# Optimization experiments

Measured on AMD Instinct MI355X. Metric: run time of the kernel, lower is better.

Reference implementation:

```python
import jax, jax.numpy as jnp
import numpy as np

EMBED_DIM = 1024
NUM_HEADS = 16
HEAD_DIM = EMBED_DIM // NUM_HEADS
B, SQ, SKV = 2, 2048, 2048


def setup_inputs() -> dict:
    key = jax.random.key(0)
    ks = jax.random.split(key, 12)
    s = 1.0 / np.sqrt(EMBED_DIM)
    inp = {
        "query": jax.random.normal(ks[0], (B, SQ, EMBED_DIM), jnp.float32),
        "key": jax.random.normal(ks[1], (B, SKV, EMBED_DIM), jnp.float32),
        "value": jax.random.normal(ks[2], (B, SKV, EMBED_DIM), jnp.float32),
        "Wq": jax.random.normal(ks[3], (EMBED_DIM, EMBED_DIM), jnp.float32) * s,
        "bq": jnp.zeros((EMBED_DIM,), jnp.float32),
        "Wk": jax.random.normal(ks[4], (EMBED_DIM, EMBED_DIM), jnp.float32) * s,
        "bk": jnp.zeros((EMBED_DIM,), jnp.float32),
        "Wv": jax.random.normal(ks[5], (EMBED_DIM, EMBED_DIM), jnp.float32) * s,
        "bv": jnp.zeros((EMBED_DIM,), jnp.float32),
        "Wo": jax.random.normal(ks[6], (EMBED_DIM, EMBED_DIM), jnp.float32) * s,
        "bo": jnp.zeros((EMBED_DIM,), jnp.float32),
        "ln_gamma": jnp.ones((EMBED_DIM,), jnp.float32),
        "ln_beta": jnp.zeros((EMBED_DIM,), jnp.float32),
    }
    return inp


def reference(query, key, value, Wq, bq, Wk, bk, Wv, bv, Wo, bo, ln_gamma, ln_beta):
    b, sq, d = query.shape
    skv = key.shape[1]
    residual = query
    # projections -> [b, h, s, hd]
    Q = (query @ Wq + bq).reshape(b, sq, NUM_HEADS, HEAD_DIM).transpose(0, 2, 1, 3)
    K = (key @ Wk + bk).reshape(b, skv, NUM_HEADS, HEAD_DIM).transpose(0, 2, 1, 3)
    V = (value @ Wv + bv).reshape(b, skv, NUM_HEADS, HEAD_DIM).transpose(0, 2, 1, 3)
    scores = jnp.einsum("bhqd,bhkd->bhqk", Q, K) / jnp.sqrt(jnp.float32(HEAD_DIM)).astype(Q.dtype)
    attn = jax.nn.softmax(scores, axis=-1)  # dropout identity in eval
    attended = jnp.einsum("bhqk,bhkd->bhqd", attn, V)
    attended = attended.transpose(0, 2, 1, 3).reshape(b, sq, d)
    out = attended @ Wo + bo
    x = out + residual
    mu = jnp.mean(x, axis=-1, keepdims=True)
    var = jnp.var(x, axis=-1, keepdims=True)
    return (x - mu) / jnp.sqrt(var + 1e-5) * ln_gamma + ln_beta
```

## Files before the change

kernel.cpp:

```cpp
#include <hip/hip_runtime.h>

#define EMBED 1024
#define NHEAD 16
#define HDIM  64
#define BATCH 2
#define SEQ   2048
#define ROWS  (BATCH*SEQ)

typedef __bf16 bf16x8 __attribute__((ext_vector_type(8)));
typedef float  f32x4  __attribute__((ext_vector_type(4)));
typedef float  f32x16 __attribute__((ext_vector_type(16)));
typedef unsigned short u16x8 __attribute__((ext_vector_type(8)));
typedef unsigned short u16x4 __attribute__((ext_vector_type(4)));
typedef unsigned int   u32x2 __attribute__((ext_vector_type(2)));

__device__ __forceinline__ unsigned short f2bf(float f) {
    unsigned int u = __float_as_uint(f);
    u += 0x7FFFu + ((u >> 16) & 1u);
    return (unsigned short)(u >> 16);
}
__device__ __forceinline__ f32x4 zero4() { f32x4 z = {0.f, 0.f, 0.f, 0.f}; return z; }

__device__ __forceinline__ unsigned int cvtpk_bf16(float lo, float hi) {
    unsigned int r;
    asm("v_cvt_pk_bf16_f32 %0, %1, %2" : "=v"(r) : "v"(lo), "v"(hi));
    return r;
}
__device__ __forceinline__ void pl32swap(unsigned int &a, unsigned int &b) {
    asm("v_permlane32_swap_b32 %0, %1" : "+v"(a), "+v"(b));
}
__device__ __forceinline__ float exp2_hw(float x) {
    float r;
    asm("v_exp_f32 %0, %1" : "=v"(r) : "v"(x));
    return r;
}

__device__ __forceinline__ void gl_lds16(const unsigned short* g, unsigned short* l) {
    __builtin_amdgcn_global_load_lds(
        (const __attribute__((address_space(1))) void*)g,
        (__attribute__((address_space(3))) void*)l, 16, 0, 0);
}

__global__ __launch_bounds__(256) void cvt3_kernel(const float* __restrict__ q,
                                                   const float* __restrict__ k,
                                                   const float* __restrict__ v,
                                                   unsigned short* __restrict__ qo,
                                                   unsigned short* __restrict__ ko,
                                                   unsigned short* __restrict__ vo) {
    const float* in; unsigned short* out;
    if (blockIdx.y == 0)      { in = q; out = qo; }
    else if (blockIdx.y == 1) { in = k; out = ko; }
    else                      { in = v; out = vo; }
    int i = (blockIdx.x * 256 + threadIdx.x) * 4;
    float4 vv = *(const float4*)(in + i);
    u16x4 o = {f2bf(vv.x), f2bf(vv.y), f2bf(vv.z), f2bf(vv.w)};
    *(u16x4*)(out + i) = o;
}

__global__ __launch_bounds__(256) void transpose4_kernel(const float* __restrict__ w0,
                                                         const float* __restrict__ w1,
                                                         const float* __restrict__ w2,
                                                         const float* __restrict__ w3,
                                                         unsigned short* __restrict__ o0,
                                                         unsigned short* __restrict__ o1,
                                                         unsigned short* __restrict__ o2,
                                                         unsigned short* __restrict__ o3) {
    const float* in; unsigned short* out;
    if (blockIdx.z == 0)      { in = w0; out = o0; }
    else if (blockIdx.z == 1) { in = w1; out = o1; }
    else if (blockIdx.z == 2) { in = w2; out = o2; }
    else                      { in = w3; out = o3; }
    __shared__ float tile[32][33];
    int tx = threadIdx.x, ty = threadIdx.y;
    int x = blockIdx.x * 32 + tx;
    int y0 = blockIdx.y * 32 + ty;
#pragma unroll
    for (int r = 0; r < 4; ++r)
        tile[ty + 8 * r][tx] = in[(size_t)(y0 + 8 * r) * EMBED + x];
    __syncthreads();
    int ox = blockIdx.y * 32 + tx;
    int oy = blockIdx.x * 32 + ty;
#pragma unroll
    for (int r = 0; r < 4; ++r)
        out[(size_t)(oy + 8 * r) * EMBED + ox] = f2bf(tile[tx][ty + 8 * r]);
}

__global__ __launch_bounds__(256, 2) void gemm_qkv_kernel(
    const unsigned short* __restrict__ qb, const unsigned short* __restrict__ kb,
    const unsigned short* __restrict__ vb,
    const unsigned short* __restrict__ Wqt, const unsigned short* __restrict__ Wkt,
    const unsigned short* __restrict__ Wvt,
    const float* __restrict__ bq, const float* __restrict__ bk, const float* __restrict__ bv,
    unsigned short* __restrict__ Qp, unsigned short* __restrict__ Kp,
    unsigned short* __restrict__ Vtb) {
    __shared__ unsigned short smem[16384];
    const unsigned short *A, *Bt; const float* bias; unsigned short* outp; int mode; float osc;
    if (blockIdx.z == 0)      { A = qb; Bt = Wqt; bias = bq; outp = Qp;  mode = 0; osc = 0.18033688f; }
    else if (blockIdx.z == 1) { A = kb; Bt = Wkt; bias = bk; outp = Kp;  mode = 0; osc = 1.0f; }
    else                      { A = vb; Bt = Wvt; bias = bv; outp = Vtb; mode = 1; osc = 1.0f; }

    const int t = threadIdx.x;
    const int m0 = blockIdx.x * 128, n0 = blockIdx.y * 128;
    const int wave = t >> 6, lane = t & 63;
    const int wr = wave >> 1, wc = wave & 1;
    const int lm = lane & 15, lq = lane >> 4;
    const int sr = t >> 2;
    const int csrc = (t & 3) ^ ((sr >> 1) & 3);
    const int pa = lq ^ ((lm >> 1) & 3);

    const unsigned short* gA = A + (size_t)(m0 + sr) * EMBED + csrc * 8;
    const unsigned short* gB = Bt + (size_t)(n0 + sr) * EMBED + csrc * 8;

    f32x4 acc[4][4];
#pragma unroll
    for (int i = 0; i < 4; ++i)
#pragma unroll
        for (int j = 0; j < 4; ++j) acc[i][j] = zero4();

    gl_lds16(gA,              smem + wave * 512);
    gl_lds16(gA + 64 * EMBED, smem + 2048 + wave * 512);
    gl_lds16(gB,              smem + 8192 + wave * 512);
    gl_lds16(gB + 64 * EMBED, smem + 8192 + 2048 + wave * 512);
    gA += 32; gB += 32;
    gl_lds16(gA,              smem + 4096 + wave * 512);
    gl_lds16(gA + 64 * EMBED, smem + 4096 + 2048 + wave * 512);
    gl_lds16(gB,              smem + 8192 + 4096 + wave * 512);
    gl_lds16(gB + 64 * EMBED, smem + 8192 + 4096 + 2048 + wave * 512);
    gA += 32; gB += 32;

    for (int kk = 0; kk < 32; ++kk) {
        if (kk < 31) { asm volatile("s_waitcnt vmcnt(4)" ::: "memory"); }
        else         { asm volatile("s_waitcnt vmcnt(0)" ::: "memory"); }
        __builtin_amdgcn_s_barrier();
        const int cbo = (kk & 1) * 4096;
        bf16x8 af[4], bfr[4];
#pragma unroll
        for (int i = 0; i < 4; ++i)
            af[i] = *(const bf16x8*)&smem[cbo + (wr * 64 + i * 16 + lm) * 32 + pa * 8];
#pragma unroll
        for (int j = 0; j < 4; ++j)
            bfr[j] = *(const bf16x8*)&smem[8192 + cbo + (wc * 64 + j * 16 + lm) * 32 + pa * 8];
#pragma unroll
        for (int i = 0; i < 4; ++i)
#pragma unroll
            for (int j = 0; j < 4; ++j)
                acc[i][j] = __builtin_amdgcn_mfma_f32_16x16x32_bf16(af[i], bfr[j], acc[i][j], 0, 0, 0);
        if (kk < 30) {
            __builtin_amdgcn_s_barrier();
            gl_lds16(gA,              smem + cbo + wave * 512);
            gl_lds16(gA + 64 * EMBED, smem + cbo + 2048 + wave * 512);
            gl_lds16(gB,              smem + 8192 + cbo + wave * 512);
            gl_lds16(gB + 64 * EMBED, smem + 8192 + cbo + 2048 + wave * 512);
            gA += 32; gB += 32;
        }
    }

    const int row = t >> 2, seg = t & 3;
    if (mode == 0) {
#pragma unroll
        for (int p = 0; p < 2; ++p) {
            __syncthreads();
            if (wr == p) {
#pragma unroll
                for (int i = 0; i < 4; ++i)
#pragma unroll
                    for (int j = 0; j < 4; ++j) {
                        float bn = bias[n0 + wc * 64 + j * 16 + lm];
                        int nl = wc * 64 + j * 16 + lm;
#pragma unroll
                        for (int r = 0; r < 4; ++r)
                            smem[(i * 16 + lq * 4 + r) * 136 + nl] =
                                f2bf((acc[i][j][r] + bn) * osc);
                    }
            }
            __syncthreads();
            int m = m0 + p * 64 + row;
            int b = m >> 11, sI = m & 2047;
            int ncol = n0 + seg * 32;
            int h = ncol >> 6, hd0 = ncol & 63;
            unsigned short* dst = outp + (((size_t)((b * NHEAD + h) * SEQ + sI)) << 6) + hd0;
            const unsigned short* src = smem + row * 136 + seg * 32;
            *(u16x8*)(dst)      = *(const u16x8*)(src);
            *(u16x8*)(dst + 8)  = *(const u16x8*)(src + 8);
            *(u16x8*)(dst + 16) = *(const u16x8*)(src + 16);
            *(u16x8*)(dst + 24) = *(const u16x8*)(src + 24);
        }
    } else {
#pragma unroll
        for (int p = 0; p < 2; ++p) {
            __syncthreads();
            if (wc == p) {
#pragma unroll
                for (int i = 0; i < 4; ++i)
#pragma unroll
                    for (int j = 0; j < 4; ++j) {
                        float bn = bias[n0 + p * 64 + j * 16 + lm];
                        u16x4 pw = {f2bf(acc[i][j][0] + bn), f2bf(acc[i][j][1] + bn),
                                    f2bf(acc[i][j][2] + bn), f2bf(acc[i][j][3] + bn)};
                        *(u16x4*)&smem[(j * 16 + lm) * 136 + wr * 64 + i * 16 + lq * 4] = pw;
                    }
            }
            __syncthreads();
            int n = n0 + p * 64 + row;
            int h = n >> 6, hd = n & 63;
            int b = m0 >> 11;
            int s0 = (m0 & 2047) + seg * 32;
            unsigned short* dst = outp + ((size_t)((b * NHEAD + h) * HDIM + hd)) * SEQ + s0;
            const unsigned short* src = smem + row * 136 + seg * 32;
            *(u16x8*)(dst)      = *(const u16x8*)(src);
            *(u16x8*)(dst + 8)  = *(const u16x8*)(src + 8);
            *(u16x8*)(dst + 16) = *(const u16x8*)(src + 16);
            *(u16x8*)(dst + 24) = *(const u16x8*)(src + 24);
        }
    }
}

__global__ __launch_bounds__(256, 2) void gemm_o_kernel(
    const unsigned short* __restrict__ att, const unsigned short* __restrict__ Wot,
    const float* __restrict__ bo, float* __restrict__ xbuf,
    const float* __restrict__ residual) {
    __shared__ unsigned short As[2][2048];
    __shared__ unsigned short Bs[2][4096];
    const int t = threadIdx.x;
    const int m0 = blockIdx.x * 64, n0 = blockIdx.y * 128;
    const int wave = t >> 6, lane = t & 63;
    const int lm = lane & 15, lq = lane >> 4;
    const int sr = t >> 2;
    const int csrc = (t & 3) ^ ((sr >> 1) & 3);
    const int pa = lq ^ ((lm >> 1) & 3);

    const unsigned short* gA = att + (size_t)(m0 + sr) * EMBED + csrc * 8;
    const unsigned short* gB = Wot + (size_t)(n0 + sr) * EMBED + csrc * 8;

    f32x4 acc[4][2];
#pragma unroll
    for (int i = 0; i < 4; ++i)
#pragma unroll
        for (int j = 0; j < 2; ++j) acc[i][j] = zero4();

    gl_lds16(gA,              As[0] + wave * 512);
    gl_lds16(gB,              Bs[0] + wave * 512);
    gl_lds16(gB + 64 * EMBED, Bs[0] + 2048 + wave * 512);
    gA += 32; gB += 32;
    gl_lds16(gA,              As[1] + wave * 512);
    gl_lds16(gB,              Bs[1] + wave * 512);
    gl_lds16(gB + 64 * EMBED, Bs[1] + 2048 + wave * 512);
    gA += 32; gB += 32;

    for (int kk = 0; kk < 32; ++kk) {
        if (kk < 31) { asm volatile("s_waitcnt vmcnt(3)" ::: "memory"); }
        else         { asm volatile("s_waitcnt vmcnt(0)" ::: "memory"); }
        __builtin_amdgcn_s_barrier();
        const int cb = kk & 1;
        bf16x8 af[4], bfr[2];
#pragma unroll
        for (int i = 0; i < 4; ++i)
            af[i] = *(const bf16x8*)&As[cb][(i * 16 + lm) * 32 + pa * 8];
#pragma unroll
        for (int j = 0; j < 2; ++j)
            bfr[j] = *(const bf16x8*)&Bs[cb][(wave * 32 + j * 16 + lm) * 32 + pa * 8];
#pragma unroll
        for (int i = 0; i < 4; ++i)
#pragma unroll
            for (int j = 0; j < 2; ++j)
                acc[i][j] = __builtin_amdgcn_mfma_f32_16x16x32_bf16(af[i], bfr[j], acc[i][j], 0, 0, 0);
        if (kk < 30) {
            __builtin_amdgcn_s_barrier();
            gl_lds16(gA,              As[cb] + wave * 512);
            gl_lds16(gB,              Bs[cb] + wave * 512);
            gl_lds16(gB + 64 * EMBED, Bs[cb] + 2048 + wave * 512);
            gA += 32; gB += 32;
        }
    }

#pragma unroll
    for (int i = 0; i < 4; ++i)
#pragma unroll
        for (int j = 0; j < 2; ++j) {
            int n = n0 + wave * 32 + j * 16 + lm;
            float bn = bo[n];
#pragma unroll
            for (int r = 0; r < 4; ++r) {
                int m = m0 + i * 16 + lq * 4 + r;
                size_t idx = (size_t)m * EMBED + n;
                xbuf[idx] = acc[i][j][r] + bn + residual[idx];
            }
        }
}

__global__ __launch_bounds__(256, 2) void attn_kernel(const unsigned short* __restrict__ Qp,
                                                      const unsigned short* __restrict__ Kp,
                                                      const unsigned short* __restrict__ Vt,
                                                      unsigned short* __restrict__ att) {
    __shared__ unsigned short Ks[16384];
    __shared__ unsigned short Vs[16384];
    const int t = threadIdx.x;
    const int bh = blockIdx.x;
    const int b = bh >> 4, h = bh & 15;
    const int q0 = blockIdx.y * 128;
    const unsigned short* Qh = Qp + (size_t)bh * SEQ * HDIM;
    const unsigned short* Kh = Kp + (size_t)bh * SEQ * HDIM;
    const unsigned short* Vh = Vt + (size_t)bh * HDIM * SEQ;
    const int wave = t >> 6, lane = t & 63;
    const int ln31 = lane & 31, half = lane >> 5;

    bf16x8 qf[4];
    {
        const unsigned short* qptr = Qh + (size_t)(q0 + wave * 32 + ln31) * HDIM + half * 8;
#pragma unroll
        for (int s = 0; s < 4; ++s) qf[s] = *(const bf16x8*)(qptr + s * 16);
    }

    const int q8a = t, q8b = 256 + t;
    const int fa = q8a >> 6, fb = q8b >> 6;
    const int ma = q8a & 31, mb = q8b & 31;
    const int ha = (q8a >> 5) & 1, hb = (q8b >> 5) & 1;
    const unsigned short* gK0 = Kh + (size_t)((fa >> 2) * 32 + ma) * HDIM + (fa & 3) * 16 + ha * 8;
    const unsigned short* gK1 = Kh + (size_t)((fb >> 2) * 32 + mb) * HDIM + (fb & 3) * 16 + hb * 8;
    const unsigned short* gV0 = Vh + (size_t)((fa >> 2) * 32 + ma) * SEQ + (fa & 3) * 16 + ha * 8;
    const unsigned short* gV1 = Vh + (size_t)((fb >> 2) * 32 + mb) * SEQ + (fb & 3) * 16 + hb * 8;

    gl_lds16(gK0,              Ks + wave * 512);
    gl_lds16(gK1,              Ks + 2048 + wave * 512);
    gl_lds16(gK0 + 64 * HDIM,  Ks + 4096 + wave * 512);
    gl_lds16(gK1 + 64 * HDIM,  Ks + 4096 + 2048 + wave * 512);
    gl_lds16(gV0,              Vs + wave * 512);
    gl_lds16(gV1,              Vs + 2048 + wave * 512);
    gl_lds16(gV0 + 64,         Vs + 4096 + wave * 512);
    gl_lds16(gV1 + 64,         Vs + 4096 + 2048 + wave * 512);
    gK0 += 128 * HDIM; gK1 += 128 * HDIM; gV0 += 128; gV1 += 128;
    gl_lds16(gK0,              Ks + 8192 + wave * 512);
    gl_lds16(gK1,              Ks + 8192 + 2048 + wave * 512);
    gl_lds16(gK0 + 64 * HDIM,  Ks + 8192 + 4096 + wave * 512);
    gl_lds16(gK1 + 64 * HDIM,  Ks + 8192 + 4096 + 2048 + wave * 512);
    gl_lds16(gV0,              Vs + 8192 + wave * 512);
    gl_lds16(gV1,              Vs + 8192 + 2048 + wave * 512);
    gl_lds16(gV0 + 64,         Vs + 8192 + 4096 + wave * 512);
    gl_lds16(gV1 + 64,         Vs + 8192 + 4096 + 2048 + wave * 512);
    gK0 += 128 * HDIM; gK1 += 128 * HDIM; gV0 += 128; gV1 += 128;

    f32x16 Oa[2][2];
#pragma unroll
    for (int mo = 0; mo < 2; ++mo)
#pragma unroll
        for (int pr = 0; pr < 2; ++pr)
#pragma unroll
            for (int r = 0; r < 16; ++r) Oa[mo][pr][r] = 0.f;
    float l_run = 0.f;

    for (int kt2 = 0; kt2 < 16; ++kt2) {
        if (kt2 < 15) { asm volatile("s_waitcnt vmcnt(8)" ::: "memory"); }
        else          { asm volatile("s_waitcnt vmcnt(0)" ::: "memory"); }
        __builtin_amdgcn_s_barrier();
        const int cbo = (kt2 & 1) * 8192;

        f32x16 S[2][2];
#pragma unroll
        for (int tl = 0; tl < 2; ++tl)
#pragma unroll
            for (int mt = 0; mt < 2; ++mt)
#pragma unroll
                for (int r = 0; r < 16; ++r) S[tl][mt][r] = -17.312340f;

        __builtin_amdgcn_s_setprio(1);
#pragma unroll
        for (int tl = 0; tl < 2; ++tl)
#pragma unroll
            for (int mt = 0; mt < 2; ++mt) {
#pragma unroll
                for (int s = 0; s < 4; ++s) {
                    bf16x8 af = *(const bf16x8*)&Ks[cbo + tl * 4096 + (mt * 4 + s) * 512 + half * 256 + ln31 * 8];
                    S[tl][mt] = __builtin_amdgcn_mfma_f32_32x32x16_bf16(af, qf[s], S[tl][mt], 0, 0, 0);
                }
            }
        __builtin_amdgcn_s_setprio(0);

#pragma unroll
        for (int tl = 0; tl < 2; ++tl) {
            float rp0 = 0.f, rp1 = 0.f, rp2 = 0.f, rp3 = 0.f;
#pragma unroll
            for (int mt = 0; mt < 2; ++mt)
#pragma unroll
                for (int rg = 0; rg < 4; ++rg) {
                    float p0 = exp2_hw(S[tl][mt][rg * 4 + 0]);
                    float p1 = exp2_hw(S[tl][mt][rg * 4 + 1]);
                    float p2 = exp2_hw(S[tl][mt][rg * 4 + 2]);
                    float p3 = exp2_hw(S[tl][mt][rg * 4 + 3]);
                    S[tl][mt][rg * 4 + 0] = p0; rp0 += p0;
                    S[tl][mt][rg * 4 + 1] = p1; rp1 += p1;
                    S[tl][mt][rg * 4 + 2] = p2; rp2 += p2;
                    S[tl][mt][rg * 4 + 3] = p3; rp3 += p3;
                }
            float rs = (rp0 + rp1) + (rp2 + rp3);
            rs += __shfl_xor(rs, 32);
            l_run += rs;

            __builtin_amdgcn_s_setprio(1);
#pragma unroll
            for (int mt = 0; mt < 2; ++mt)
#pragma unroll
                for (int p = 0; p < 2; ++p) {
                    unsigned int a0 = cvtpk_bf16(S[tl][mt][8 * p + 0], S[tl][mt][8 * p + 1]);
                    unsigned int a1 = cvtpk_bf16(S[tl][mt][8 * p + 2], S[tl][mt][8 * p + 3]);
                    unsigned int b0 = cvtpk_bf16(S[tl][mt][8 * p + 4], S[tl][mt][8 * p + 5]);
                    unsigned int b1 = cvtpk_bf16(S[tl][mt][8 * p + 6], S[tl][mt][8 * p + 7]);
                    pl32swap(a0, b0);
                    pl32swap(a1, b1);
                    union { unsigned int u[4]; bf16x8 v; } bp;
                    bp.u[0] = a0; bp.u[1] = a1; bp.u[2] = b0; bp.u[3] = b1;
                    const int sp = mt * 2 + p;
#pragma unroll
                    for (int mo = 0; mo < 2; ++mo) {
                        bf16x8 av = *(const bf16x8*)&Vs[cbo + tl * 4096 + (mo * 4 + sp) * 512 + half * 256 + ln31 * 8];
                        Oa[mo][p] = __builtin_amdgcn_mfma_f32_32x32x16_bf16(av, bp.v, Oa[mo][p], 0, 0, 0);
                    }
                }
            __builtin_amdgcn_s_setprio(0);
        }

        if (kt2 < 14) {
            __builtin_amdgcn_s_barrier();
            gl_lds16(gK0,              Ks + cbo + wave * 512);
            gl_lds16(gK1,              Ks + cbo + 2048 + wave * 512);
            gl_lds16(gK0 + 64 * HDIM,  Ks + cbo + 4096 + wave * 512);
            gl_lds16(gK1 + 64 * HDIM,  Ks + cbo + 4096 + 2048 + wave * 512);
            gl_lds16(gV0,              Vs + cbo + wave * 512);
            gl_lds16(gV1,              Vs + cbo + 2048 + wave * 512);
            gl_lds16(gV0 + 64,         Vs + cbo + 4096 + wave * 512);
            gl_lds16(gV1 + 64,         Vs + cbo + 4096 + 2048 + wave * 512);
            gK0 += 128 * HDIM; gK1 += 128 * HDIM; gV0 += 128; gV1 += 128;
        }
    }

    float inv = 1.f / l_run;
    int q = q0 + wave * 32 + ln31;
    unsigned short* orow = att + (size_t)(b * SEQ + q) * EMBED + h * HDIM;
#pragma unroll
    for (int mo = 0; mo < 2; ++mo)
#pragma unroll
        for (int rg = 0; rg < 4; ++rg) {
            u16x4 ow = {f2bf((Oa[mo][0][rg * 4 + 0] + Oa[mo][1][rg * 4 + 0]) * inv),
                        f2bf((Oa[mo][0][rg * 4 + 1] + Oa[mo][1][rg * 4 + 1]) * inv),
                        f2bf((Oa[mo][0][rg * 4 + 2] + Oa[mo][1][rg * 4 + 2]) * inv),
                        f2bf((Oa[mo][0][rg * 4 + 3] + Oa[mo][1][rg * 4 + 3]) * inv)};
            *(u16x4*)&orow[mo * 32 + rg * 8 + half * 4] = ow;
        }
}

__global__ __launch_bounds__(256) void ln_kernel(const float* __restrict__ x,
                                                 const float* __restrict__ gamma,
                                                 const float* __restrict__ beta,
                                                 float* __restrict__ out) {
    __shared__ float red[8];
    const int row = blockIdx.x, t = threadIdx.x;
    float4 v = *(const float4*)(x + (size_t)row * EMBED + t * 4);
    float s = v.x + v.y + v.z + v.w;
    float ss = v.x * v.x + v.y * v.y + v.z * v.z + v.w * v.w;
#pragma unroll
    for (int o = 1; o < 64; o <<= 1) {
        s += __shfl_xor(s, o);
        ss += __shfl_xor(ss, o);
    }
    int wave = t >> 6, lane = t & 63;
    if (lane == 0) { red[wave] = s; red[4 + wave] = ss; }
    __syncthreads();
    s = red[0] + red[1] + red[2] + red[3];
    ss = red[4] + red[5] + red[6] + red[7];
    float mu = s * (1.f / EMBED);
    float var = ss * (1.f / EMBED) - mu * mu;
    float rstd = rsqrtf(var + 1e-5f);
    float4 g = *(const float4*)(gamma + t * 4);
    float4 bb = *(const float4*)(beta + t * 4);
    float4 o;
    o.x = (v.x - mu) * rstd * g.x + bb.x;
    o.y = (v.y - mu) * rstd * g.y + bb.y;
    o.z = (v.z - mu) * rstd * g.z + bb.z;
    o.w = (v.w - mu) * rstd * g.w + bb.w;
    *(float4*)(out + (size_t)row * EMBED + t * 4) = o;
}

extern "C" void kernel_launch(void* const* d_in, const int* in_sizes, int n_in,
                              void* d_out, int out_size, void* d_ws, size_t ws_size,
                              hipStream_t stream) {
    const float* query = (const float*)d_in[0];
    const float* key_  = (const float*)d_in[1];
    const float* value = (const float*)d_in[2];
    const float* Wq = (const float*)d_in[3];
    const float* bq = (const float*)d_in[4];
    const float* Wk = (const float*)d_in[5];
    const float* bk = (const float*)d_in[6];
    const float* Wv = (const float*)d_in[7];
    const float* bv = (const float*)d_in[8];
    const float* Wo = (const float*)d_in[9];
    const float* bo = (const float*)d_in[10];
    const float* gamma = (const float*)d_in[11];
    const float* beta  = (const float*)d_in[12];

    char* ws = (char*)d_ws;
    const size_t MB = 1024 * 1024;
    unsigned short* qb  = (unsigned short*)(ws + 0);
    unsigned short* kb  = (unsigned short*)(ws + 8 * MB);
    unsigned short* vb  = (unsigned short*)(ws + 16 * MB);
    unsigned short* Wqt = (unsigned short*)(ws + 24 * MB);
    unsigned short* Wkt = (unsigned short*)(ws + 26 * MB);
    unsigned short* Wvt = (unsigned short*)(ws + 28 * MB);
    unsigned short* Wot = (unsigned short*)(ws + 30 * MB);
    unsigned short* Qp  = (unsigned short*)(ws + 32 * MB);
    unsigned short* Kp  = (unsigned short*)(ws + 40 * MB);
    unsigned short* Vtb = (unsigned short*)(ws + 48 * MB);
    unsigned short* att = (unsigned short*)(ws + 0);
    float*          xbuf = (float*)(ws + 8 * MB);

    cvt3_kernel<<<dim3(4096, 3), 256, 0, stream>>>(query, key_, value, qb, kb, vb);
    transpose4_kernel<<<dim3(32, 32, 4), dim3(32, 8), 0, stream>>>(Wq, Wk, Wv, Wo, Wqt, Wkt, Wvt, Wot);

    gemm_qkv_kernel<<<dim3(32, 8, 3), 256, 0, stream>>>(qb, kb, vb, Wqt, Wkt, Wvt,
                                                        bq, bk, bv, Qp, Kp, Vtb);

    attn_kernel<<<dim3(32, 16), 256, 0, stream>>>(Qp, Kp, Vtb, att);

    gemm_o_kernel<<<dim3(64, 8), 256, 0, stream>>>(att, Wot, bo, xbuf, query);
    ln_kernel<<<ROWS, 256, 0, stream>>>(xbuf, gamma, beta, (float*)d_out);
}
```

Before: 232.2 us.

## Triple-buffer GEMM LDS pipelines and defer softmax row-sum reduction in attention

Both projection GEMMs go from double to triple LDS buffering. The next stage's global-to-LDS load is now issued before the current tile's MFMAs, and the second barrier per iteration is removed. In the attention kernel, the constant score offset is folded into the first MFMA's accumulator input, and the per-tile cross-lane row-sum shuffle is replaced by four running partial sums reduced once at the end with a permlane swap. The extra LDS in the GEMMs may reduce occupancy, and keeping the partial sums longer adds register pressure.

```diff
diff --git a/kernel.cpp b/kernel.cpp
--- a/kernel.cpp
+++ b/kernel.cpp
@@ -12,7 +12,6 @@
 typedef float  f32x16 __attribute__((ext_vector_type(16)));
 typedef unsigned short u16x8 __attribute__((ext_vector_type(8)));
 typedef unsigned short u16x4 __attribute__((ext_vector_type(4)));
-typedef unsigned int   u32x2 __attribute__((ext_vector_type(2)));
 
 __device__ __forceinline__ unsigned short f2bf(float f) {
     unsigned int u = __float_as_uint(f);
@@ -93,7 +92,7 @@
     const float* __restrict__ bq, const float* __restrict__ bk, const float* __restrict__ bv,
     unsigned short* __restrict__ Qp, unsigned short* __restrict__ Kp,
     unsigned short* __restrict__ Vtb) {
-    __shared__ unsigned short smem[16384];
+    __shared__ unsigned short smem[24576];
     const unsigned short *A, *Bt; const float* bias; unsigned short* outp; int mode; float osc;
     if (blockIdx.z == 0)      { A = qb; Bt = Wqt; bias = bq; outp = Qp;  mode = 0; osc = 0.18033688f; }
     else if (blockIdx.z == 1) { A = kb; Bt = Wkt; bias = bk; outp = Kp;  mode = 0; osc = 1.0f; }
@@ -117,43 +116,52 @@
 #pragma unroll
         for (int j = 0; j < 4; ++j) acc[i][j] = zero4();
 
-    gl_lds16(gA,              smem + wave * 512);
-    gl_lds16(gA + 64 * EMBED, smem + 2048 + wave * 512);
-    gl_lds16(gB,              smem + 8192 + wave * 512);
-    gl_lds16(gB + 64 * EMBED, smem + 8192 + 2048 + wave * 512);
+#define QKV_STAGE(SOFF)                                                      \
+    gl_lds16(gA,              smem + (SOFF) + wave * 512);                   \
+    gl_lds16(gA + 64 * EMBED, smem + (SOFF) + 2048 + wave * 512);            \
+    gl_lds16(gB,              smem + 12288 + (SOFF) + wave * 512);           \
+    gl_lds16(gB + 64 * EMBED, smem + 12288 + (SOFF) + 2048 + wave * 512);    \
     gA += 32; gB += 32;
-    gl_lds16(gA,              smem + 4096 + wave * 512);
-    gl_lds16(gA + 64 * EMBED, smem + 4096 + 2048 + wave * 512);
-    gl_lds16(gB,              smem + 8192 + 4096 + wave * 512);
-    gl_lds16(gB + 64 * EMBED, smem + 8192 + 4096 + 2048 + wave * 512);
-    gA += 32; gB += 32;
-
-    for (int kk = 0; kk < 32; ++kk) {
-        if (kk < 31) { asm volatile("s_waitcnt vmcnt(4)" ::: "memory"); }
-        else         { asm volatile("s_waitcnt vmcnt(0)" ::: "memory"); }
-        __builtin_amdgcn_s_barrier();
-        const int cbo = (kk & 1) * 4096;
-        bf16x8 af[4], bfr[4];
-#pragma unroll
-        for (int i = 0; i < 4; ++i)
-            af[i] = *(const bf16x8*)&smem[cbo + (wr * 64 + i * 16 + lm) * 32 + pa * 8];
-#pragma unroll
-        for (int j = 0; j < 4; ++j)
-            bfr[j] = *(const bf16x8*)&smem[8192 + cbo + (wc * 64 + j * 16 + lm) * 32 + pa * 8];
-#pragma unroll
-        for (int i = 0; i < 4; ++i)
-#pragma unroll
-            for (int j = 0; j < 4; ++j)
-                acc[i][j] = __builtin_amdgcn_mfma_f32_16x16x32_bf16(af[i], bfr[j], acc[i][j], 0, 0, 0);
-        if (kk < 30) {
-            __builtin_amdgcn_s_barrier();
-            gl_lds16(gA,              smem + cbo + wave * 512);
-            gl_lds16(gA + 64 * EMBED, smem + cbo + 2048 + wave * 512);
-            gl_lds16(gB,              smem + 8192 + cbo + wave * 512);
-            gl_lds16(gB + 64 * EMBED, smem + 8192 + cbo + 2048 + wave * 512);
-            gA += 32; gB += 32;
-        }
-    }
+
+#define QKV_COMP(COFF)                                                                 \
+    {                                                                                  \
+        bf16x8 af[4], bfr[4];                                                          \
+        _Pragma("unroll")                                                              \
+        for (int i = 0; i < 4; ++i)                                                    \
+            af[i] = *(const bf16x8*)&smem[(COFF) + (wr * 64 + i * 16 + lm) * 32 + pa * 8]; \
+        _Pragma("unroll")                                                              \
+        for (int j = 0; j < 4; ++j)                                                    \
+            bfr[j] = *(const bf16x8*)&smem[12288 + (COFF) + (wc * 64 + j * 16 + lm) * 32 + pa * 8]; \
+        _Pragma("unroll")                                                              \
+        for (int i = 0; i < 4; ++i)                                                    \
+            _Pragma("unroll")                                                          \
+            for (int j = 0; j < 4; ++j)                                                \
+                acc[i][j] = __builtin_amdgcn_mfma_f32_16x16x32_bf16(af[i], bfr[j], acc[i][j], 0, 0, 0); \
+    }
+
+    QKV_STAGE(0)
+    QKV_STAGE(4096)
+
+    for (int g = 0; g < 10; ++g) {
+        asm volatile("s_waitcnt vmcnt(4)" ::: "memory");
+        __builtin_amdgcn_s_barrier();
+        QKV_STAGE(8192)
+        QKV_COMP(0)
+        asm volatile("s_waitcnt vmcnt(4)" ::: "memory");
+        __builtin_amdgcn_s_barrier();
+        QKV_STAGE(0)
+        QKV_COMP(4096)
+        asm volatile("s_waitcnt vmcnt(4)" ::: "memory");
+        __builtin_amdgcn_s_barrier();
+        QKV_STAGE(4096)
+        QKV_COMP(8192)
+    }
+    asm volatile("s_waitcnt vmcnt(4)" ::: "memory");
+    __builtin_amdgcn_s_barrier();
+    QKV_COMP(0)
+    asm volatile("s_waitcnt vmcnt(0)" ::: "memory");
+    __builtin_amdgcn_s_barrier();
+    QKV_COMP(4096)
 
     const int row = t >> 2, seg = t & 3;
     if (mode == 0) {
@@ -213,14 +221,15 @@
             *(u16x8*)(dst + 24) = *(const u16x8*)(src + 24);
         }
     }
+#undef QKV_STAGE
+#undef QKV_COMP
 }
 
 __global__ __launch_bounds__(256, 2) void gemm_o_kernel(
     const unsigned short* __restrict__ att, const unsigned short* __restrict__ Wot,
     const float* __restrict__ bo, float* __restrict__ xbuf,
     const float* __restrict__ residual) {
-    __shared__ unsigned short As[2][2048];
-    __shared__ unsigned short Bs[2][4096];
+    __shared__ unsigned short smem[18432];
     const int t = threadIdx.x;
     const int m0 = blockIdx.x * 64, n0 = blockIdx.y * 128;
     const int wave = t >> 6, lane = t & 63;
@@ -238,40 +247,51 @@
 #pragma unroll
         for (int j = 0; j < 2; ++j) acc[i][j] = zero4();
 
-    gl_lds16(gA,              As[0] + wave * 512);
-    gl_lds16(gB,              Bs[0] + wave * 512);
-    gl_lds16(gB + 64 * EMBED, Bs[0] + 2048 + wave * 512);
+#define O_STAGE(SA, SB)                                                  \
+    gl_lds16(gA,              smem + (SA) + wave * 512);                 \
+    gl_lds16(gB,              smem + 6144 + (SB) + wave * 512);          \
+    gl_lds16(gB + 64 * EMBED, smem + 6144 + (SB) + 2048 + wave * 512);   \
     gA += 32; gB += 32;
-    gl_lds16(gA,              As[1] + wave * 512);
-    gl_lds16(gB,              Bs[1] + wave * 512);
-    gl_lds16(gB + 64 * EMBED, Bs[1] + 2048 + wave * 512);
-    gA += 32; gB += 32;
-
-    for (int kk = 0; kk < 32; ++kk) {
-        if (kk < 31) { asm volatile("s_waitcnt vmcnt(3)" ::: "memory"); }
-        else         { asm volatile("s_waitcnt vmcnt(0)" ::: "memory"); }
-        __builtin_amdgcn_s_barrier();
-        const int cb = kk & 1;
-        bf16x8 af[4], bfr[2];
-#pragma unroll
-        for (int i = 0; i < 4; ++i)
-            af[i] = *(const bf16x8*)&As[cb][(i * 16 + lm) * 32 + pa * 8];
-#pragma unroll
-        for (int j = 0; j < 2; ++j)
-            bfr[j] = *(const bf16x8*)&Bs[cb][(wave * 32 + j * 16 + lm) * 32 + pa * 8];
-#pragma unroll
-        for (int i = 0; i < 4; ++i)
-#pragma unroll
-            for (int j = 0; j < 2; ++j)
-                acc[i][j] = __builtin_amdgcn_mfma_f32_16x16x32_bf16(af[i], bfr[j], acc[i][j], 0, 0, 0);
-        if (kk < 30) {
-            __builtin_amdgcn_s_barrier();
-            gl_lds16(gA,              As[cb] + wave * 512);
-            gl_lds16(gB,              Bs[cb] + wave * 512);
-            gl_lds16(gB + 64 * EMBED, Bs[cb] + 2048 + wave * 512);
-            gA += 32; gB += 32;
-        }
-    }
+
+#define O_COMP(SA, SB)                                                                \
+    {                                                                                 \
+        bf16x8 af[4], bfr[2];                                                         \
+        _Pragma("unroll")                                                             \
+        for (int i = 0; i < 4; ++i)                                                   \
+            af[i] = *(const bf16x8*)&smem[(SA) + (i * 16 + lm) * 32 + pa * 8];        \
+        _Pragma("unroll")                                                             \
+        for (int j = 0; j < 2; ++j)                                                   \
+            bfr[j] = *(const bf16x8*)&smem[6144 + (SB) + (wave * 32 + j * 16 + lm) * 32 + pa * 8]; \
+        _Pragma("unroll")                                                             \
+        for (int i = 0; i < 4; ++i)                                                   \
+            _Pragma("unroll")                                                         \
+            for (int j = 0; j < 2; ++j)                                               \
+                acc[i][j] = __builtin_amdgcn_mfma_f32_16x16x32_bf16(af[i], bfr[j], acc[i][j], 0, 0, 0); \
+    }
+
+    O_STAGE(0, 0)
+    O_STAGE(2048, 4096)
+
+    for (int g = 0; g < 10; ++g) {
+        asm volatile("s_waitcnt vmcnt(3)" ::: "memory");
+        __builtin_amdgcn_s_barrier();
+        O_STAGE(4096, 8192)
+        O_COMP(0, 0)
+        asm volatile("s_waitcnt vmcnt(3)" ::: "memory");
+        __builtin_amdgcn_s_barrier();
+        O_STAGE(0, 0)
+        O_COMP(2048, 4096)
+        asm volatile("s_waitcnt vmcnt(3)" ::: "memory");
+        __builtin_amdgcn_s_barrier();
+        O_STAGE(2048, 4096)
+        O_COMP(4096, 8192)
+    }
+    asm volatile("s_waitcnt vmcnt(3)" ::: "memory");
+    __builtin_amdgcn_s_barrier();
+    O_COMP(0, 0)
+    asm volatile("s_waitcnt vmcnt(0)" ::: "memory");
+    __builtin_amdgcn_s_barrier();
+    O_COMP(2048, 4096)
 
 #pragma unroll
     for (int i = 0; i < 4; ++i)
@@ -286,6 +306,8 @@
                 xbuf[idx] = acc[i][j][r] + bn + residual[idx];
             }
         }
+#undef O_STAGE
+#undef O_COMP
 }
 
 __global__ __launch_bounds__(256, 2) void attn_kernel(const unsigned short* __restrict__ Qp,
@@ -339,6 +361,10 @@
     gl_lds16(gV1 + 64,         Vs + 8192 + 4096 + 2048 + wave * 512);
     gK0 += 128 * HDIM; gK1 += 128 * HDIM; gV0 += 128; gV1 += 128;
 
+    f32x16 OFFS;
+#pragma unroll
+    for (int r = 0; r < 16; ++r) OFFS[r] = -17.312340f;
+
     f32x16 Oa[2][2];
 #pragma unroll
     for (int mo = 0; mo < 2; ++mo)
@@ -346,7 +372,7 @@
         for (int pr = 0; pr < 2; ++pr)
 #pragma unroll
             for (int r = 0; r < 16; ++r) Oa[mo][pr][r] = 0.f;
-    float l_run = 0.f;
+    float rpA = 0.f, rpB = 0.f, rpC = 0.f, rpD = 0.f;
 
     for (int kt2 = 0; kt2 < 16; ++kt2) {
         if (kt2 < 15) { asm volatile("s_waitcnt vmcnt(8)" ::: "memory"); }
@@ -355,20 +381,17 @@
         const int cbo = (kt2 & 1) * 8192;
 
         f32x16 S[2][2];
+        __builtin_amdgcn_s_setprio(1);
 #pragma unroll
         for (int tl = 0; tl < 2; ++tl)
 #pragma unroll
-            for (int mt = 0; mt < 2; ++mt)
-#pragma unroll
-                for (int r = 0; r < 16; ++r) S[tl][mt][r] = -17.312340f;
-
-        __builtin_amdgcn_s_setprio(1);
-#pragma unroll
-        for (int tl = 0; tl < 2; ++tl)
-#pragma unroll
             for (int mt = 0; mt < 2; ++mt) {
-#pragma unroll
-                for (int s = 0; s < 4; ++s) {
+                {
+                    bf16x8 af = *(const bf16x8*)&Ks[cbo + tl * 4096 + (mt * 4 + 0) * 512 + half * 256 + ln31 * 8];
+                    S[tl][mt] = __builtin_amdgcn_mfma_f32_32x32x16_bf16(af, qf[0], OFFS, 0, 0, 0);
+                }
+#pragma unroll
+                for (int s = 1; s < 4; ++s) {
                     bf16x8 af = *(const bf16x8*)&Ks[cbo + tl * 4096 + (mt * 4 + s) * 512 + half * 256 + ln31 * 8];
                     S[tl][mt] = __builtin_amdgcn_mfma_f32_32x32x16_bf16(af, qf[s], S[tl][mt], 0, 0, 0);
                 }
@@ -377,7 +400,6 @@
 
 #pragma unroll
         for (int tl = 0; tl < 2; ++tl) {
-            float rp0 = 0.f, rp1 = 0.f, rp2 = 0.f, rp3 = 0.f;
 #pragma unroll
             for (int mt = 0; mt < 2; ++mt)
 #pragma unroll
@@ -386,14 +408,11 @@
                     float p1 = exp2_hw(S[tl][mt][rg * 4 + 1]);
                     float p2 = exp2_hw(S[tl][mt][rg * 4 + 2]);
                     float p3 = exp2_hw(S[tl][mt][rg * 4 + 3]);
-                    S[tl][mt][rg * 4 + 0] = p0; rp0 += p0;
-                    S[tl][mt][rg * 4 + 1] = p1; rp1 += p1;
-                    S[tl][mt][rg * 4 + 2] = p2; rp2 += p2;
-                    S[tl][mt][rg * 4 + 3] = p3; rp3 += p3;
+                    S[tl][mt][rg * 4 + 0] = p0; rpA += p0;
+                    S[tl][mt][rg * 4 + 1] = p1; rpB += p1;
+                    S[tl][mt][rg * 4 + 2] = p2; rpC += p2;
+                    S[tl][mt][rg * 4 + 3] = p3; rpD += p3;
                 }
-            float rs = (rp0 + rp1) + (rp2 + rp3);
-            rs += __shfl_xor(rs, 32);
-            l_run += rs;
 
             __builtin_amdgcn_s_setprio(1);
 #pragma unroll
@@ -432,7 +451,11 @@
         }
     }
 
-    float inv = 1.f / l_run;
+    float l_loc = (rpA + rpB) + (rpC + rpD);
+    unsigned int la = __float_as_uint(l_loc), lb = __float_as_uint(l_loc);
+    pl32swap(la, lb);
+    float inv = 1.f / (__uint_as_float(la) + __uint_as_float(lb));
+
     int q = q0 + wave * 32 + ln31;
     unsigned short* orow = att + (size_t)(b * SEQ + q) * EMBED + h * HDIM;
 #pragma unroll
```

Measured after the change: 227.4 us. 1.02x faster.
